# Kernel tuning notes

Hardware: AMD Instinct MI355X
Metric: run time of the kernel (lower is better)

The kernel has to match this reference:

```python
import jax, jax.numpy as jnp
import numpy as np

B, T, C = 4, 4096, 1024
HEAD = 128


def setup_inputs() -> dict:
    key = jax.random.key(0)
    k0, k1, k2, k3 = jax.random.split(key, 4)
    x = jax.random.normal(k0, (B, T, C), dtype=jnp.float32)
    # bias-free linear weights, stored as (in, out) so y = x @ W
    Wk = jax.random.normal(k1, (C, HEAD), dtype=jnp.float32) * (C ** -0.5)
    Wq = jax.random.normal(k2, (C, HEAD), dtype=jnp.float32) * (C ** -0.5)
    Wv = jax.random.normal(k3, (C, HEAD), dtype=jnp.float32) * (C ** -0.5)
    return {"x": x, "Wk": Wk, "Wq": Wq, "Wv": Wv}


def reference(x, Wk, Wq, Wv):
    Bx, Tx, Cx = x.shape
    k = x @ Wk            # [B,T,H]
    q = x @ Wq            # [B,T,H]
    v = x @ Wv            # [B,T,H]
    # NOTE: original code scales by C**-0.5 where C = n_embd (input dim), not head_size
    scale = Cx ** -0.5
    wei = jnp.einsum("bqh,bkh->bqk", q, k) * scale        # [B,T,T]
    causal = jnp.arange(Tx)[:, None] >= jnp.arange(Tx)[None, :]
    wei = jnp.where(causal, wei, -jnp.inf)
    wei = jax.nn.softmax(wei, axis=-1)
    # dropout rate is 0.0 in the source -> identity
    return jnp.einsum("bqk,bkh->bqh", wei, v)             # [B,T,H]
```

## Files before the change

kernel.cpp:

```cpp
#include <hip/hip_runtime.h>


typedef __bf16 bf16;
typedef bf16 bf16x8 __attribute__((ext_vector_type(8)));
typedef bf16 bf16x4 __attribute__((ext_vector_type(4)));
typedef float f32x4 __attribute__((ext_vector_type(4)));

#define L2E 1.4426950408889634f
#define TSEQ 4096
#define CDIM 1024
#define HDIM 128
#define MROWS 16384

#define GLDS(g, l)                                              \
  __builtin_amdgcn_global_load_lds(                             \
      (__attribute__((address_space(1))) void*)(g),             \
      (__attribute__((address_space(3))) void*)(l), 16, 0, 0)

static __device__ inline unsigned pkbf(float a, float b) {
  union { bf16 h; unsigned short u; } ua, ub;
  ua.h = (bf16)a; ub.h = (bf16)b;
  return ((unsigned)ub.u << 16) | (unsigned)ua.u;
}

__global__ __launch_bounds__(256) void wt_prep(const float* __restrict__ Wq,
                                               const float* __restrict__ Wk,
                                               const float* __restrict__ Wv,
                                               bf16* __restrict__ WT) {
  const int mode = blockIdx.y;
  const float* W = (mode == 0) ? Wq : (mode == 1) ? Wk : Wv;
  const int idx = blockIdx.x * 256 + threadIdx.x;
  const int n = idx >> 10;
  const int k = idx & 1023;
  WT[(size_t)mode * 131072 + idx] = (bf16)W[(size_t)k * HDIM + n];
}

__global__ __launch_bounds__(256) void qkv_gemm(const float* __restrict__ x,
                                                const bf16* __restrict__ WT,
                                                bf16* __restrict__ qb,
                                                bf16* __restrict__ kb,
                                                bf16* __restrict__ vT) {
  __shared__ __attribute__((aligned(16))) bf16 a_tile[128 * 32];
  __shared__ __attribute__((aligned(16))) bf16 b_tile[128 * 32];
  const int tid = threadIdx.x;
  const int wid = tid >> 6;
  const int lane = tid & 63;
  const int lr = lane & 15;
  const int lg = lane >> 4;
  const int wr = wid >> 1;
  const int wc = wid & 1;
  const int mode = blockIdx.y;
  const int m0 = blockIdx.x * 128;
  const bf16* wt = WT + (size_t)mode * 131072;

  int rowA[2], col8[2];
#pragma unroll
  for (int g = 0; g < 2; ++g) {
    const int idx8 = g * 256 + tid;
    rowA[g] = idx8 >> 2;
    col8[g] = (idx8 & 3) * 8;
  }

  f32x4 acc[4][4] = {};

  float4 fA[2][2];
  bf16x8 fB[2];
#pragma unroll
  for (int g = 0; g < 2; ++g) {
    const float* src = x + (size_t)(m0 + rowA[g]) * CDIM + col8[g];
    fA[g][0] = *(const float4*)src;
    fA[g][1] = *(const float4*)(src + 4);
    fB[g] = *(const bf16x8*)(wt + (size_t)rowA[g] * CDIM + col8[g]);
  }

#pragma unroll 1
  for (int kt = 0; kt < 32; ++kt) {
    __syncthreads();
#pragma unroll
    for (int g = 0; g < 2; ++g) {
      bf16x8 av;
      av[0] = (bf16)fA[g][0].x; av[1] = (bf16)fA[g][0].y;
      av[2] = (bf16)fA[g][0].z; av[3] = (bf16)fA[g][0].w;
      av[4] = (bf16)fA[g][1].x; av[5] = (bf16)fA[g][1].y;
      av[6] = (bf16)fA[g][1].z; av[7] = (bf16)fA[g][1].w;
      *(bf16x8*)&a_tile[rowA[g] * 32 + col8[g]] = av;
      *(bf16x8*)&b_tile[rowA[g] * 32 + col8[g]] = fB[g];
    }
    __syncthreads();
    if (kt + 1 < 32) {
#pragma unroll
      for (int g = 0; g < 2; ++g) {
        const float* src = x + (size_t)(m0 + rowA[g]) * CDIM + (kt + 1) * 32 + col8[g];
        fA[g][0] = *(const float4*)src;
        fA[g][1] = *(const float4*)(src + 4);
        fB[g] = *(const bf16x8*)(wt + (size_t)rowA[g] * CDIM + (kt + 1) * 32 + col8[g]);
      }
    }
    bf16x8 af[4], bfr[4];
#pragma unroll
    for (int r = 0; r < 4; ++r)
      af[r] = *(const bf16x8*)&a_tile[(wr * 64 + r * 16 + lr) * 32 + lg * 8];
#pragma unroll
    for (int c = 0; c < 4; ++c)
      bfr[c] = *(const bf16x8*)&b_tile[(wc * 64 + c * 16 + lr) * 32 + lg * 8];
#pragma unroll
    for (int r = 0; r < 4; ++r)
#pragma unroll
      for (int c = 0; c < 4; ++c)
        acc[r][c] = __builtin_amdgcn_mfma_f32_16x16x32_bf16(af[r], bfr[c], acc[r][c], 0, 0, 0);
  }

  if (mode < 2) {
    bf16* dst = (mode == 0) ? qb : kb;
    const float sc = (mode == 0) ? 0.03125f : 1.0f;
#pragma unroll
    for (int r = 0; r < 4; ++r)
#pragma unroll
      for (int c = 0; c < 4; ++c)
#pragma unroll
        for (int j = 0; j < 4; ++j) {
          const int row = m0 + wr * 64 + r * 16 + lg * 4 + j;
          const int col = wc * 64 + c * 16 + lr;
          dst[(size_t)row * HDIM + col] = (bf16)(acc[r][c][j] * sc);
        }
  } else {
#pragma unroll
    for (int r = 0; r < 4; ++r)
#pragma unroll
      for (int c = 0; c < 4; ++c) {
        const int row0 = m0 + wr * 64 + r * 16 + lg * 4;
        const int col = wc * 64 + c * 16 + lr;
        bf16x4 pv;
        pv[0] = (bf16)acc[r][c][0]; pv[1] = (bf16)acc[r][c][1];
        pv[2] = (bf16)acc[r][c][2]; pv[3] = (bf16)acc[r][c][3];
        *(bf16x4*)(vT + (size_t)col * MROWS + row0) = pv;
      }
  }
}

__global__ __launch_bounds__(512, 4) void attn_part(const bf16* __restrict__ qg,
                                                    const bf16* __restrict__ kb,
                                                    const bf16* __restrict__ vT,
                                                    bf16* __restrict__ po,
                                                    float* __restrict__ pm,
                                                    float* __restrict__ pl,
                                                    int cshift, int maxc) {
  __shared__ __attribute__((aligned(16))) char kv_lds[2][32768];
  __shared__ __attribute__((aligned(16))) bf16 p_lds[8][16][64];
  const int tid = threadIdx.x;
  const int wid = tid >> 6;
  const int lane = tid & 63;
  const int lr = lane & 15;
  const int lg = lane >> 4;
  const int b = blockIdx.z;
  const int c = blockIdx.y;
  const int qbase = blockIdx.x * 128;
  const int kv0 = c << cshift;
  if (kv0 >= qbase + 128) return;
  const int kvend = min(kv0 + (1 << cshift), qbase + 128);
  const int nt = (kvend - kv0) >> 6;
  const int qr0 = qbase + wid * 16;
  const int grp = blockIdx.x * 8 + wid;
  const size_t qrow = (size_t)b * TSEQ + qr0;

  const int wbase = wid * 2048;
  int ksrc[2], vsrc[2];
#pragma unroll
  for (int i = 0; i < 2; ++i) {
    const int o = wbase + i * 1024 + lane * 16;
    const int rk = o >> 8;
    ksrc[i] = rk * 256 + ((o & 255) ^ ((rk & 7) << 4));
    const int rv = o >> 7;
    vsrc[i] = rv * (MROWS * 2) + ((o & 127) ^ ((rv & 7) << 4));
  }
  const char* kgb = (const char*)kb + (size_t)b * TSEQ * 256;
  const char* vgb = (const char*)vT + (size_t)b * TSEQ * 2;

  const int msk = (lr & 7) << 4;
  const int m30 = (lr & 3) << 4;
  const int m6 = (lr & 4) << 4;
  const int lgx = (lg * 16) ^ m30;
  const int kreadA = lr * 256 + lgx + m6;
  const int kreadB = lr * 256 + lgx + (64 ^ m6);
  const int vreadA = 16384 + lr * 128 + lgx + m6;
  const int vreadB = 16384 + lr * 128 + lgx + (64 ^ m6);

  bf16x8 qf[4];
#pragma unroll
  for (int d = 0; d < 4; ++d)
    qf[d] = *(const bf16x8*)(qg + (qrow + lr) * HDIM + d * 32 + lg * 8);

  f32x4 o_[8] = {};
  float m_ = -1e30f, l_ = 0.0f;

  {
    const char* ks = kgb + (size_t)kv0 * 256;
    const char* vs = vgb + (size_t)kv0 * 2;
#pragma unroll
    for (int i = 0; i < 2; ++i) {
      GLDS(ks + ksrc[i], &kv_lds[0][wbase + i * 1024]);
      GLDS(vs + vsrc[i], &kv_lds[0][16384 + wbase + i * 1024]);
    }
  }
  __syncthreads();

  int cur = 0;
  for (int t = 0; t < nt; ++t) {
    const int kvt = kv0 + (t << 6);
    if (t + 1 < nt) {
      const char* ks = kgb + (size_t)(kvt + 64) * 256;
      const char* vs = vgb + (size_t)(kvt + 64) * 2;
#pragma unroll
      for (int i = 0; i < 2; ++i) {
        GLDS(ks + ksrc[i], &kv_lds[cur ^ 1][wbase + i * 1024]);
        GLDS(vs + vsrc[i], &kv_lds[cur ^ 1][16384 + wbase + i * 1024]);
      }
    }
    if (kvt < qr0 + 16) {
      const char* kbuf = kv_lds[cur];
      f32x4 s[4] = {};
      __builtin_amdgcn_s_setprio(1);
#pragma unroll
      for (int nf = 0; nf < 4; ++nf) {
        const char* kb0 = kbuf + nf * 4096;
        bf16x8 kf;
        kf = *(const bf16x8*)(kb0 + kreadA);
        s[nf] = __builtin_amdgcn_mfma_f32_16x16x32_bf16(kf, qf[0], s[nf], 0, 0, 0);
        kf = *(const bf16x8*)(kb0 + kreadB);
        s[nf] = __builtin_amdgcn_mfma_f32_16x16x32_bf16(kf, qf[1], s[nf], 0, 0, 0);
        kf = *(const bf16x8*)(kb0 + kreadA + 128);
        s[nf] = __builtin_amdgcn_mfma_f32_16x16x32_bf16(kf, qf[2], s[nf], 0, 0, 0);
        kf = *(const bf16x8*)(kb0 + kreadB + 128);
        s[nf] = __builtin_amdgcn_mfma_f32_16x16x32_bf16(kf, qf[3], s[nf], 0, 0, 0);
      }
      __builtin_amdgcn_s_setprio(0);
      if (kvt + 63 >= qr0) {
        const int q = qr0 + lr;
#pragma unroll
        for (int nf = 0; nf < 4; ++nf)
#pragma unroll
          for (int j = 0; j < 4; ++j)
            if (kvt + nf * 16 + lg * 4 + j > q) s[nf][j] = -1e30f;
      }
      float rmax = fmaxf(fmaxf(s[0][0], s[0][1]), fmaxf(s[0][2], s[0][3]));
#pragma unroll
      for (int nf = 1; nf < 4; ++nf)
        rmax = fmaxf(rmax, fmaxf(fmaxf(s[nf][0], s[nf][1]), fmaxf(s[nf][2], s[nf][3])));
      rmax = fmaxf(rmax, __shfl_xor(rmax, 16));
      rmax = fmaxf(rmax, __shfl_xor(rmax, 32));
      if (!__all(rmax <= m_ + 8.0f)) {
        const float mn = fmaxf(m_, rmax);
        const float al = exp2f((m_ - mn) * L2E);
        m_ = mn;
        l_ *= al;
#pragma unroll
        for (int o = 0; o < 8; ++o)
#pragma unroll
          for (int j = 0; j < 4; ++j) o_[o][j] *= al;
      }
      float rsum = 0.0f;
#pragma unroll
      for (int nf = 0; nf < 4; ++nf)
#pragma unroll
        for (int j = 0; j < 4; ++j) {
          s[nf][j] = exp2f((s[nf][j] - m_) * L2E);
          rsum += s[nf][j];
        }
      {
        char* pw = (char*)p_lds + wid * 2048 + lr * 128;
#pragma unroll
        for (int nf = 0; nf < 4; ++nf) {
          uint2 w2;
          w2.x = pkbf(s[nf][0], s[nf][1]); w2.y = pkbf(s[nf][2], s[nf][3]);
          *(uint2*)(pw + (((nf * 32) + lg * 8) ^ msk)) = w2;
        }
      }
      rsum += __shfl_xor(rsum, 16); rsum += __shfl_xor(rsum, 32); l_ += rsum;
      asm volatile("s_waitcnt lgkmcnt(0)" ::: "memory");
      __builtin_amdgcn_sched_barrier(0);
      const char* pr = (const char*)p_lds + wid * 2048 + lr * 128;
      bf16x8 pf0 = *(const bf16x8*)(pr + lgx + m6);
      bf16x8 pf1 = *(const bf16x8*)(pr + lgx + (64 ^ m6));
      __builtin_amdgcn_s_setprio(1);
#pragma unroll
      for (int o = 0; o < 8; ++o) {
        bf16x8 vf;
        vf = *(const bf16x8*)(kbuf + vreadA + o * 2048);
        o_[o] = __builtin_amdgcn_mfma_f32_16x16x32_bf16(vf, pf0, o_[o], 0, 0, 0);
        vf = *(const bf16x8*)(kbuf + vreadB + o * 2048);
        o_[o] = __builtin_amdgcn_mfma_f32_16x16x32_bf16(vf, pf1, o_[o], 0, 0, 0);
      }
      __builtin_amdgcn_s_setprio(0);
    }
    __syncthreads();
    cur ^= 1;
  }

  const size_t slot = (size_t)(b * 256 + grp) * maxc + c;
  bf16* pob = po + slot * (16 * HDIM);
#pragma unroll
  for (int o = 0; o < 8; ++o) {
    bf16x4 pv;
    pv[0] = (bf16)o_[o][0]; pv[1] = (bf16)o_[o][1];
    pv[2] = (bf16)o_[o][2]; pv[3] = (bf16)o_[o][3];
    *(bf16x4*)(pob + lr * HDIM + o * 16 + lg * 4) = pv;
  }
  if (lg == 0) {
    pm[slot * 16 + lr] = m_;
    pl[slot * 16 + lr] = l_;
  }
}

__global__ __launch_bounds__(256) void attn_merge(const bf16* __restrict__ po,
                                                  const float* __restrict__ pm,
                                                  const float* __restrict__ pl,
                                                  float* __restrict__ out,
                                                  int cshift, int maxc) {
  const int bg = blockIdx.x;
  const int g = bg & 255;
  const int nch = ((g << 4) >> cshift) + 1;
  const int row = threadIdx.x >> 4;
  const int d8 = (threadIdx.x & 15) * 8;
  const size_t slot0 = (size_t)bg * maxc;

  float M = -1e30f;
  for (int c = 0; c < nch; ++c) M = fmaxf(M, pm[(slot0 + c) * 16 + row]);
  float L = 0.0f;
  float acc[8] = {};
  for (int c = 0; c < nch; ++c) {
    const float w = exp2f((pm[(slot0 + c) * 16 + row] - M) * L2E);
    L += w * pl[(slot0 + c) * 16 + row];
    const bf16x8 v = *(const bf16x8*)(po + (slot0 + c) * (16 * HDIM) + row * HDIM + d8);
#pragma unroll
    for (int i = 0; i < 8; ++i) acc[i] += w * (float)v[i];
  }
  const float inv = 1.0f / L;
  f32x4 r0, r1;
#pragma unroll
  for (int i = 0; i < 4; ++i) { r0[i] = acc[i] * inv; r1[i] = acc[i + 4] * inv; }
  float* dst = out + (size_t)bg * (16 * HDIM) + row * HDIM + d8;
  *(f32x4*)dst = r0;
  *(f32x4*)(dst + 4) = r1;
}

extern "C" void kernel_launch(void* const* d_in, const int* in_sizes, int n_in,
                              void* d_out, int out_size, void* d_ws, size_t ws_size,
                              hipStream_t stream) {
  const float* x  = (const float*)d_in[0];
  const float* Wk = (const float*)d_in[1];
  const float* Wq = (const float*)d_in[2];
  const float* Wv = (const float*)d_in[3];
  float* out = (float*)d_out;

  char* ws = (char*)d_ws;
  bf16* qb = (bf16*)(ws);
  bf16* kb = (bf16*)(ws + 4194304);
  bf16* vT = (bf16*)(ws + 8388608);
  bf16* WT = (bf16*)(ws + 12582912);
  const size_t pbase = 13369344;

  int cshift, maxc;
  if (ws_size >= pbase + 8ull * 1024 * 4224) { cshift = 9;  maxc = 8; }
  else if (ws_size >= pbase + 4ull * 1024 * 4224) { cshift = 10; maxc = 4; }
  else { cshift = 12; maxc = 1; }
  bf16* po = (bf16*)(ws + pbase);
  float* pm = (float*)(ws + pbase + (size_t)maxc * 1024 * 16 * 128 * 2);
  float* pl = pm + (size_t)maxc * 1024 * 16;

  wt_prep<<<dim3(512, 3), 256, 0, stream>>>(Wq, Wk, Wv, WT);
  qkv_gemm<<<dim3(128, 3), 256, 0, stream>>>(x, WT, qb, kb, vT);
  attn_part<<<dim3(32, maxc, 4), 512, 0, stream>>>(qb, kb, vT, po, pm, pl, cshift, maxc);
  attn_merge<<<1024, 256, 0, stream>>>(po, pm, pl, out, cshift, maxc);
}
```

Before: 100.7 us.

## Fuse QKV projections into one GEMM and triple-buffer attention KV loads

The QKV GEMM now computes all three projections in one block over a 64-row tile of x, so each fp32 x tile is loaded and converted once rather than three times. Weight tiles are streamed with direct global-to-LDS loads. The attention kernel moves from double to triple-buffered K/V tiles, prefetching two tiles ahead and syncing with vmcnt waits plus raw barriers instead of __syncthreads. The extra LDS lowers the occupancy hint from 4 to 2 blocks per CU, and the fused GEMM launches fewer but heavier blocks.

```diff
diff --git a/kernel.cpp b/kernel.cpp
--- a/kernel.cpp
+++ b/kernel.cpp
@@ -35,13 +35,13 @@
   WT[(size_t)mode * 131072 + idx] = (bf16)W[(size_t)k * HDIM + n];
 }
 
-__global__ __launch_bounds__(256) void qkv_gemm(const float* __restrict__ x,
-                                                const bf16* __restrict__ WT,
-                                                bf16* __restrict__ qb,
-                                                bf16* __restrict__ kb,
-                                                bf16* __restrict__ vT) {
-  __shared__ __attribute__((aligned(16))) bf16 a_tile[128 * 32];
-  __shared__ __attribute__((aligned(16))) bf16 b_tile[128 * 32];
+__global__ __launch_bounds__(256) void qkv_fused(const float* __restrict__ x,
+                                                 const bf16* __restrict__ WT,
+                                                 bf16* __restrict__ qb,
+                                                 bf16* __restrict__ kb,
+                                                 bf16* __restrict__ vT) {
+  __shared__ __attribute__((aligned(16))) bf16 a_tile[64 * 32];
+  __shared__ __attribute__((aligned(16))) bf16 b_tile[384 * 32];
   const int tid = threadIdx.x;
   const int wid = tid >> 6;
   const int lane = tid & 63;
@@ -49,103 +49,90 @@
   const int lg = lane >> 4;
   const int wr = wid >> 1;
   const int wc = wid & 1;
-  const int mode = blockIdx.y;
-  const int m0 = blockIdx.x * 128;
-  const bf16* wt = WT + (size_t)mode * 131072;
-
-  int rowA[2], col8[2];
-#pragma unroll
-  for (int g = 0; g < 2; ++g) {
-    const int idx8 = g * 256 + tid;
-    rowA[g] = idx8 >> 2;
-    col8[g] = (idx8 & 3) * 8;
-  }
-
-  f32x4 acc[4][4] = {};
-
-  float4 fA[2][2];
-  bf16x8 fB[2];
-#pragma unroll
-  for (int g = 0; g < 2; ++g) {
-    const float* src = x + (size_t)(m0 + rowA[g]) * CDIM + col8[g];
-    fA[g][0] = *(const float4*)src;
-    fA[g][1] = *(const float4*)(src + 4);
-    fB[g] = *(const bf16x8*)(wt + (size_t)rowA[g] * CDIM + col8[g]);
+  const int m0 = blockIdx.x * 64;
+
+  const int ra = tid >> 2;
+  const int ca = (tid & 3) * 8;
+  int bn[6], bc[6];
+#pragma unroll
+  for (int i = 0; i < 6; ++i) {
+    const int db = (i * 4 + wid) * 1024 + lane * 16;
+    bn[i] = db >> 6;
+    bc[i] = db & 63;
+  }
+
+  f32x4 acc[2][12] = {};
+  float4 a0, a1;
+  {
+    const float* s = x + (size_t)(m0 + ra) * CDIM + ca;
+    a0 = *(const float4*)s;
+    a1 = *(const float4*)(s + 4);
   }
 
 #pragma unroll 1
   for (int kt = 0; kt < 32; ++kt) {
     __syncthreads();
-#pragma unroll
-    for (int g = 0; g < 2; ++g) {
+    {
       bf16x8 av;
-      av[0] = (bf16)fA[g][0].x; av[1] = (bf16)fA[g][0].y;
-      av[2] = (bf16)fA[g][0].z; av[3] = (bf16)fA[g][0].w;
-      av[4] = (bf16)fA[g][1].x; av[5] = (bf16)fA[g][1].y;
-      av[6] = (bf16)fA[g][1].z; av[7] = (bf16)fA[g][1].w;
-      *(bf16x8*)&a_tile[rowA[g] * 32 + col8[g]] = av;
-      *(bf16x8*)&b_tile[rowA[g] * 32 + col8[g]] = fB[g];
+      av[0] = (bf16)a0.x; av[1] = (bf16)a0.y; av[2] = (bf16)a0.z; av[3] = (bf16)a0.w;
+      av[4] = (bf16)a1.x; av[5] = (bf16)a1.y; av[6] = (bf16)a1.z; av[7] = (bf16)a1.w;
+      *(bf16x8*)&a_tile[ra * 32 + ca] = av;
+    }
+#pragma unroll
+    for (int i = 0; i < 6; ++i) {
+      const char* src = (const char*)WT + (size_t)bn[i] * 2048 + kt * 64 + bc[i];
+      GLDS(src, (char*)b_tile + (i * 4 + wid) * 1024 + lane * 16);
     }
     __syncthreads();
     if (kt + 1 < 32) {
-#pragma unroll
-      for (int g = 0; g < 2; ++g) {
-        const float* src = x + (size_t)(m0 + rowA[g]) * CDIM + (kt + 1) * 32 + col8[g];
-        fA[g][0] = *(const float4*)src;
-        fA[g][1] = *(const float4*)(src + 4);
-        fB[g] = *(const bf16x8*)(wt + (size_t)rowA[g] * CDIM + (kt + 1) * 32 + col8[g]);
-      }
-    }
-    bf16x8 af[4], bfr[4];
-#pragma unroll
-    for (int r = 0; r < 4; ++r)
-      af[r] = *(const bf16x8*)&a_tile[(wr * 64 + r * 16 + lr) * 32 + lg * 8];
-#pragma unroll
-    for (int c = 0; c < 4; ++c)
-      bfr[c] = *(const bf16x8*)&b_tile[(wc * 64 + c * 16 + lr) * 32 + lg * 8];
-#pragma unroll
-    for (int r = 0; r < 4; ++r)
-#pragma unroll
-      for (int c = 0; c < 4; ++c)
-        acc[r][c] = __builtin_amdgcn_mfma_f32_16x16x32_bf16(af[r], bfr[c], acc[r][c], 0, 0, 0);
-  }
-
-  if (mode < 2) {
-    bf16* dst = (mode == 0) ? qb : kb;
-    const float sc = (mode == 0) ? 0.03125f : 1.0f;
-#pragma unroll
-    for (int r = 0; r < 4; ++r)
-#pragma unroll
-      for (int c = 0; c < 4; ++c)
-#pragma unroll
-        for (int j = 0; j < 4; ++j) {
-          const int row = m0 + wr * 64 + r * 16 + lg * 4 + j;
-          const int col = wc * 64 + c * 16 + lr;
-          dst[(size_t)row * HDIM + col] = (bf16)(acc[r][c][j] * sc);
-        }
-  } else {
-#pragma unroll
-    for (int r = 0; r < 4; ++r)
-#pragma unroll
-      for (int c = 0; c < 4; ++c) {
-        const int row0 = m0 + wr * 64 + r * 16 + lg * 4;
-        const int col = wc * 64 + c * 16 + lr;
+      const float* s = x + (size_t)(m0 + ra) * CDIM + (kt + 1) * 32 + ca;
+      a0 = *(const float4*)s;
+      a1 = *(const float4*)(s + 4);
+    }
+    bf16x8 af[2];
+#pragma unroll
+    for (int r = 0; r < 2; ++r)
+      af[r] = *(const bf16x8*)&a_tile[(wr * 32 + r * 16 + lr) * 32 + lg * 8];
+#pragma unroll
+    for (int n = 0; n < 12; ++n) {
+      bf16x8 bfr = *(const bf16x8*)&b_tile[(wc * 192 + n * 16 + lr) * 32 + lg * 8];
+      acc[0][n] = __builtin_amdgcn_mfma_f32_16x16x32_bf16(af[0], bfr, acc[0][n], 0, 0, 0);
+      acc[1][n] = __builtin_amdgcn_mfma_f32_16x16x32_bf16(af[1], bfr, acc[1][n], 0, 0, 0);
+    }
+  }
+
+#pragma unroll
+  for (int r = 0; r < 2; ++r) {
+    const int row0 = m0 + wr * 32 + r * 16 + lg * 4;
+#pragma unroll
+    for (int n = 0; n < 12; ++n) {
+      const int cg = wc * 192 + n * 16;
+      const int mode = cg >> 7;
+      const int col = (cg & 127) + lr;
+      if (mode < 2) {
+        bf16* dst = (mode == 0) ? qb : kb;
+        const float sc = (mode == 0) ? 0.03125f : 1.0f;
+#pragma unroll
+        for (int j = 0; j < 4; ++j)
+          dst[(size_t)(row0 + j) * HDIM + col] = (bf16)(acc[r][n][j] * sc);
+      } else {
         bf16x4 pv;
-        pv[0] = (bf16)acc[r][c][0]; pv[1] = (bf16)acc[r][c][1];
-        pv[2] = (bf16)acc[r][c][2]; pv[3] = (bf16)acc[r][c][3];
+        pv[0] = (bf16)acc[r][n][0]; pv[1] = (bf16)acc[r][n][1];
+        pv[2] = (bf16)acc[r][n][2]; pv[3] = (bf16)acc[r][n][3];
         *(bf16x4*)(vT + (size_t)col * MROWS + row0) = pv;
       }
-  }
-}
-
-__global__ __launch_bounds__(512, 4) void attn_part(const bf16* __restrict__ qg,
+    }
+  }
+}
+
+__global__ __launch_bounds__(512, 2) void attn_part(const bf16* __restrict__ qg,
                                                     const bf16* __restrict__ kb,
                                                     const bf16* __restrict__ vT,
                                                     bf16* __restrict__ po,
                                                     float* __restrict__ pm,
                                                     float* __restrict__ pl,
                                                     int cshift, int maxc) {
-  __shared__ __attribute__((aligned(16))) char kv_lds[2][32768];
+  __shared__ __attribute__((aligned(16))) char kv_lds[3][32768];
   __shared__ __attribute__((aligned(16))) bf16 p_lds[8][16][64];
   const int tid = threadIdx.x;
   const int wid = tid >> 6;
@@ -189,6 +176,7 @@
 #pragma unroll
   for (int d = 0; d < 4; ++d)
     qf[d] = *(const bf16x8*)(qg + (qrow + lr) * HDIM + d * 32 + lg * 8);
+  asm volatile("s_waitcnt vmcnt(0)" ::: "memory");
 
   f32x4 o_[8] = {};
   float m_ = -1e30f, l_ = 0.0f;
@@ -202,22 +190,25 @@
       GLDS(vs + vsrc[i], &kv_lds[0][16384 + wbase + i * 1024]);
     }
   }
-  __syncthreads();
-
-  int cur = 0;
+  if (nt > 1) {
+    const char* ks = kgb + (size_t)(kv0 + 64) * 256;
+    const char* vs = vgb + (size_t)(kv0 + 64) * 2;
+#pragma unroll
+    for (int i = 0; i < 2; ++i) {
+      GLDS(ks + ksrc[i], &kv_lds[1][wbase + i * 1024]);
+      GLDS(vs + vsrc[i], &kv_lds[1][16384 + wbase + i * 1024]);
+    }
+  }
+
+#pragma unroll 1
   for (int t = 0; t < nt; ++t) {
+    if (t + 1 < nt) asm volatile("s_waitcnt vmcnt(4)" ::: "memory");
+    else            asm volatile("s_waitcnt vmcnt(0)" ::: "memory");
+    __builtin_amdgcn_s_barrier();
+    __builtin_amdgcn_sched_barrier(0);
     const int kvt = kv0 + (t << 6);
-    if (t + 1 < nt) {
-      const char* ks = kgb + (size_t)(kvt + 64) * 256;
-      const char* vs = vgb + (size_t)(kvt + 64) * 2;
-#pragma unroll
-      for (int i = 0; i < 2; ++i) {
-        GLDS(ks + ksrc[i], &kv_lds[cur ^ 1][wbase + i * 1024]);
-        GLDS(vs + vsrc[i], &kv_lds[cur ^ 1][16384 + wbase + i * 1024]);
-      }
-    }
     if (kvt < qr0 + 16) {
-      const char* kbuf = kv_lds[cur];
+      const char* kbuf = kv_lds[t % 3];
       f32x4 s[4] = {};
       __builtin_amdgcn_s_setprio(1);
 #pragma unroll
@@ -292,8 +283,17 @@
       }
       __builtin_amdgcn_s_setprio(0);
     }
-    __syncthreads();
-    cur ^= 1;
+    if (t + 2 < nt) {
+      const int kvn = kv0 + ((t + 2) << 6);
+      char* db = kv_lds[(t + 2) % 3];
+      const char* ks = kgb + (size_t)kvn * 256;
+      const char* vs = vgb + (size_t)kvn * 2;
+#pragma unroll
+      for (int i = 0; i < 2; ++i) {
+        GLDS(ks + ksrc[i], db + wbase + i * 1024);
+        GLDS(vs + vsrc[i], db + 16384 + wbase + i * 1024);
+      }
+    }
   }
 
   const size_t slot = (size_t)(b * 256 + grp) * maxc + c;
@@ -368,7 +368,7 @@
   float* pl = pm + (size_t)maxc * 1024 * 16;
 
   wt_prep<<<dim3(512, 3), 256, 0, stream>>>(Wq, Wk, Wv, WT);
-  qkv_gemm<<<dim3(128, 3), 256, 0, stream>>>(x, WT, qb, kb, vT);
+  qkv_fused<<<256, 256, 0, stream>>>(x, WT, qb, kb, vT);
   attn_part<<<dim3(32, maxc, 4), 512, 0, stream>>>(qb, kb, vT, po, pm, pl, cshift, maxc);
   attn_merge<<<1024, 256, 0, stream>>>(po, pm, pl, out, cshift, maxc);
 }
```

Result: slower. 123.7 us (+22.9%).
